# Performance work log

Measured on AMD Instinct MI355X. Metric: run time of the kernel, lower is better.

## Reference

```python
import jax, jax.numpy as jnp
import numpy as np

V, E, H, A, B, S = 32000, 1024, 1024, 1024, 64, 512

def setup_inputs() -> dict:
    key = jax.random.key(0)
    ks = jax.random.split(key, 20)
    sc = lambda d: 1.0 / np.sqrt(d)
    return {
        "x": jax.random.randint(ks[0], (B,), 0, V),
        "encoder_outputs": jax.random.normal(ks[1], (S, B, H), jnp.float32),
        "h0": jax.random.normal(ks[2], (1, B, H), jnp.float32),
        "c0": jax.random.normal(ks[3], (1, B, H), jnp.float32),
        "Wa": jax.random.normal(ks[4], (A, H), jnp.float32) * sc(H),
        "b_wa": jnp.zeros((A,), jnp.float32),
        "Ua": jax.random.normal(ks[5], (A, H), jnp.float32) * sc(H),
        "b_ua": jnp.zeros((A,), jnp.float32),
        "va": jax.random.normal(ks[6], (1, A), jnp.float32) * sc(A),
        "b_va": jnp.zeros((1,), jnp.float32),
        "emb": jax.random.normal(ks[7], (V, E), jnp.float32) * 0.02,
        "W_ih": jax.random.normal(ks[8], (4 * H, E + H), jnp.float32) * sc(E + H),
        "W_hh": jax.random.normal(ks[9], (4 * H, H), jnp.float32) * sc(H),
        "b_ih": jnp.zeros((4 * H,), jnp.float32),
        "b_hh": jnp.zeros((4 * H,), jnp.float32),
        "W_clf": jax.random.normal(ks[10], (V, H), jnp.float32) * sc(H),
        "b_clf": jnp.zeros((V,), jnp.float32),
    }

def reference(x, encoder_outputs, h0, c0, Wa, b_wa, Ua, b_ua, va, b_va, emb,
              W_ih, W_hh, b_ih, b_hh, W_clf, b_clf):
    # Bahdanau additive attention: scores over time (axis 0)
    tmp1 = jnp.einsum('lbh,ah->lba', h0, Wa) + b_wa            # [1,B,A]
    tmp2 = jnp.einsum('sbh,ah->sba', encoder_outputs, Ua) + b_ua  # [S,B,A]
    scores = jnp.einsum('sba,oa->sbo', jnp.tanh(tmp1 + tmp2), va) + b_va  # [S,B,1]
    w = jax.nn.softmax(scores, axis=0)                          # softmax over S
    ctx = jnp.einsum('sb,sbh->bh', w[..., 0], encoder_outputs)  # [B,H]
    # embed token, concat with context
    inp = jnp.concatenate([emb[x], ctx], axis=-1)               # [B,E+H]
    # single LSTM step (PyTorch gate order i,f,g,o)
    gates = inp @ W_ih.T + b_ih + h0[0] @ W_hh.T + b_hh         # [B,4H]
    i, f, g, o = jnp.split(gates, 4, axis=-1)
    c1 = jax.nn.sigmoid(f) * c0[0] + jax.nn.sigmoid(i) * jnp.tanh(g)
    h1 = jax.nn.sigmoid(o) * jnp.tanh(c1)
    logits = h1 @ W_clf.T + b_clf                               # [B,V]
    return jax.nn.log_softmax(logits, axis=-1)[None]            # [1,B,V]
```

## Files before the change

### kernel.cpp

```cpp
#include <hip/hip_runtime.h>
#include <hip/hip_bf16.h>
#include <math.h>

typedef unsigned short u16;
typedef unsigned int u32;
typedef __attribute__((ext_vector_type(4))) float f32x4;
typedef __attribute__((ext_vector_type(8))) short s16x8;
typedef __attribute__((ext_vector_type(8))) unsigned short u16x8;

#define DEV __device__ __forceinline__


DEV u16 f2bf(float f) {
    union { float f; u32 u; } x{f};
    return (u16)((x.u + 0x7FFFu + ((x.u >> 16) & 1u)) >> 16);
}
DEV float bf2f(u16 h) {
    union { u32 u; float f; } x;
    x.u = ((u32)h) << 16;
    return x.f;
}
DEV float sigm(float x) { return 1.0f / (1.0f + __expf(-x)); }
DEV float tanh_f(float x) {
    float c = fminf(fmaxf(x, -9.0f), 9.0f);
    float e = __expf(2.0f * c);
    return (e - 1.0f) / (e + 1.0f);
}

#define GLL16(g, l) __builtin_amdgcn_global_load_lds( \
    (const __attribute__((address_space(1))) u32*)(g), \
    (__attribute__((address_space(3))) u32*)(l), 16, 0, 0)

__global__ __launch_bounds__(256) void kprepcvt(
    const float* __restrict__ enc, const float* __restrict__ Ua,
    const float* __restrict__ h0, u16* __restrict__ encbf,
    u16* __restrict__ Uabf, u16* __restrict__ h0bf, float* __restrict__ scores)
{
    int bid = blockIdx.x, t = threadIdx.x;
    if (bid < 16384) {
        int i = bid * 256 + t;
        float4 f0 = ((const float4*)enc)[i * 2];
        float4 f1 = ((const float4*)enc)[i * 2 + 1];
        u16x8 o = {f2bf(f0.x), f2bf(f0.y), f2bf(f0.z), f2bf(f0.w),
                   f2bf(f1.x), f2bf(f1.y), f2bf(f1.z), f2bf(f1.w)};
        ((u16x8*)encbf)[i] = o;
    } else if (bid < 16400) {
        int i = (bid - 16384) * 2048 + t * 8;
        *(float4*)(scores + i) = (float4){0.f, 0.f, 0.f, 0.f};
        *(float4*)(scores + i + 4) = (float4){0.f, 0.f, 0.f, 0.f};
    } else if (bid < 16912) {
        int i = (bid - 16400) * 256 + t;
        float4 f0 = ((const float4*)Ua)[i * 2];
        float4 f1 = ((const float4*)Ua)[i * 2 + 1];
        u16x8 o = {f2bf(f0.x), f2bf(f0.y), f2bf(f0.z), f2bf(f0.w),
                   f2bf(f1.x), f2bf(f1.y), f2bf(f1.z), f2bf(f1.w)};
        ((u16x8*)Uabf)[i] = o;
    } else {
        int i = (bid - 16912) * 256 + t;
        float4 f0 = ((const float4*)h0)[i * 2];
        float4 f1 = ((const float4*)h0)[i * 2 + 1];
        u16x8 o = {f2bf(f0.x), f2bf(f0.y), f2bf(f0.z), f2bf(f0.w),
                   f2bf(f1.x), f2bf(f1.y), f2bf(f1.z), f2bf(f1.w)};
        ((u16x8*)h0bf)[i] = o;
    }
}


template<int F0>
DEV void mmq(f32x4 (&acc)[8][4], const s16x8 (&af)[2][2], const s16x8 (&bfrag)[4][2]) {
#pragma unroll
    for (int f = 0; f < 2; f++)
#pragma unroll
        for (int j = 0; j < 4; j++) {
            acc[F0 + f][j] = __builtin_amdgcn_mfma_f32_16x16x32_bf16(af[f][0], bfrag[j][0], acc[F0 + f][j], 0, 0, 0);
            acc[F0 + f][j] = __builtin_amdgcn_mfma_f32_16x16x32_bf16(af[f][1], bfrag[j][1], acc[F0 + f][j], 0, 0, 0);
        }
}

__global__ __launch_bounds__(512, 1) void kscores256v2(
    const u16* __restrict__ encbf, const u16* __restrict__ Uabf,
    const float* __restrict__ tmp1c, const float* __restrict__ va,
    float* __restrict__ scores)
{
    __shared__ __align__(16) u16 shm[65536];

    int wg  = blockIdx.x;
    int lin = (wg & 7) * 64 + (wg >> 3);
    int mt  = lin >> 2, nt = lin & 3;

    int t = threadIdx.x;
    int wid = t >> 6, lane = t & 63;
    int wm = wid >> 2, wn = wid & 3;
    int lr = lane & 15, lg = lane >> 4;

    f32x4 acc[8][4];
#pragma unroll
    for (int i = 0; i < 8; i++)
#pragma unroll
        for (int j = 0; j < 4; j++) acc[i][j] = (f32x4){0.f, 0.f, 0.f, 0.f};

    int srow = t >> 3;
    int sq8  = ((t & 7) ^ (srow & 7)) * 8;
    const u16* asrcb = encbf + (size_t)(mt * 256 + srow) * 1024 + sq8;
    const u16* bsrcb = Uabf + (size_t)(nt * 256 + srow) * 1024 + sq8;

#define STG_A(SE, RB, KO) GLL16(asrcb + (size_t)(RB) * 1024 + (KO), shm + (SE) + (RB) * 64 + t * 8)
#define STG_B(SE, RB, KO) GLL16(bsrcb + (size_t)(RB) * 1024 + (KO), shm + (SE) + 16384 + (RB) * 64 + t * 8)

    const u16* Abase = shm + (wm * 128 + lr) * 64;
    const u16* Bbase = shm + 16384 + (wn * 64 + lr) * 64;
    int xor8 = (lr & 7) * 8;
    int o0 = (lg * 8) ^ xor8;
    int o1 = (32 + lg * 8) ^ xor8;

    s16x8 af[2][2], bfrag[4][2];

#define RD_A2(F0, AB) { \
    af[0][0] = *(const s16x8*)((AB) + (F0) * 1024 + o0); \
    af[0][1] = *(const s16x8*)((AB) + (F0) * 1024 + o1); \
    af[1][0] = *(const s16x8*)((AB) + (F0 + 1) * 1024 + o0); \
    af[1][1] = *(const s16x8*)((AB) + (F0 + 1) * 1024 + o1); }

#define MM(F0) \
    __builtin_amdgcn_s_setprio(1); \
    mmq<F0>(acc, af, bfrag); \
    __builtin_amdgcn_s_setprio(0);

#define BAR() \
    __builtin_amdgcn_s_barrier(); \
    __builtin_amdgcn_sched_barrier(0);

    STG_B(0, 0, 0);  STG_B(0, 64, 0);  STG_B(0, 128, 0); STG_B(0, 192, 0);
    STG_A(0, 0, 0);  STG_A(0, 128, 0); STG_A(0, 64, 0);  STG_A(0, 192, 0);
    STG_B(32768, 0, 64);  STG_B(32768, 64, 64);
    STG_B(32768, 128, 64); STG_B(32768, 192, 64);
    STG_A(32768, 0, 64);  STG_A(32768, 128, 64);
    asm volatile("s_waitcnt vmcnt(6)" ::: "memory");
    BAR();

#define TILE_BODY(T, SB, SBX, SAH, STP2, WC) { \
    int kA = (T) * 64 + 128; \
    int kH = (T) * 64 + 64; \
    const u16* Ab = Abase + (SB); \
    const u16* Bb = Bbase + (SB); \
     \
    if (SAH) { STG_A((SBX), 64, kH); STG_A((SBX), 192, kH); } \
    _Pragma("unroll") \
    for (int j = 0; j < 4; j++) { \
        bfrag[j][0] = *(const s16x8*)(Bb + j * 1024 + o0); \
        bfrag[j][1] = *(const s16x8*)(Bb + j * 1024 + o1); \
    } \
    RD_A2(0, Ab); \
    MM(0); \
    BAR();                       \
     \
    if (STP2) { STG_B((SB), 0, kA); STG_B((SB), 64, kA); } \
    RD_A2(2, Ab); \
    MM(2); \
    __builtin_amdgcn_sched_barrier(0); \
     \
    if (STP2) { STG_B((SB), 128, kA); STG_B((SB), 192, kA); } \
    RD_A2(4, Ab); \
    MM(4); \
    BAR();                       \
     \
    if (STP2) { STG_A((SB), 0, kA); STG_A((SB), 128, kA); } \
    RD_A2(6, Ab); \
    if ((WC) == 6) { asm volatile("s_waitcnt vmcnt(6)" ::: "memory"); } \
    else if ((WC) == 0) { asm volatile("s_waitcnt vmcnt(0)" ::: "memory"); } \
    MM(6); \
    BAR();                       \
}

    for (int tt = 0; tt < 7; tt++) {
        int T0 = tt * 2;
        TILE_BODY(T0, 0, 32768, 1, 1, 6);
        TILE_BODY(T0 + 1, 32768, 0, 1, 1, 6);
    }
    TILE_BODY(14, 0, 32768, 1, 0, 0);
    TILE_BODY(15, 32768, 0, 0, 0, -1);

    float* ltmp = (float*)shm;
#pragma unroll
    for (int i = 0; i < 8; i++) {
        int idx = t + i * 512;
        int row = idx >> 6, c4 = idx & 63;
        float4 v = *(const float4*)(tmp1c + row * 1024 + nt * 256 + c4 * 4);
        *(float4*)(ltmp + row * 260 + c4 * 4) = v;
    }
    __syncthreads();

    float vaj[4];
#pragma unroll
    for (int j = 0; j < 4; j++) vaj[j] = va[nt * 256 + wn * 64 + j * 16 + lr];

#pragma unroll
    for (int fi = 0; fi < 8; fi++) {
        float rs[4] = {0.f, 0.f, 0.f, 0.f};
#pragma unroll
        for (int j = 0; j < 4; j++) {
            int ac = wn * 64 + j * 16 + lr;
#pragma unroll
            for (int r = 0; r < 4; r++) {
                int b = (fi * 16 + lg * 4 + r) & 63;
                rs[r] += vaj[j] * tanh_f(acc[fi][j][r] + ltmp[b * 260 + ac]);
            }
        }
#pragma unroll
        for (int m = 1; m < 16; m <<= 1)
#pragma unroll
            for (int r = 0; r < 4; r++) rs[r] += __shfl_xor(rs[r], m, 64);
        if (lr == 0) {
            int mrow = mt * 256 + wm * 128 + fi * 16 + lg * 4;
#pragma unroll
            for (int r = 0; r < 4; r++) atomicAdd(&scores[mrow + r], rs[r]);
        }
    }
#undef STG_A
#undef STG_B
#undef RD_A2
#undef MM
#undef BAR
#undef TILE_BODY
}

__global__ __launch_bounds__(256) void kskinny(
    const u16* __restrict__ Abf, int Ktot,
    const float* __restrict__ B1, int K1,
    const float* __restrict__ B2,
    float* __restrict__ Cout, int N, int klen)
{
    __shared__ u16 As[64 * 40];
    __shared__ u16 Bs[128 * 40];

    int nt = blockIdx.x, p = blockIdx.y;
    int t = threadIdx.x;
    int wid = t >> 6, lane = t & 63;
    int lr = lane & 15, lg = lane >> 4;
    int K2 = Ktot - K1;

    f32x4 acc[4][2];
#pragma unroll
    for (int i = 0; i < 4; i++)
#pragma unroll
        for (int j = 0; j < 2; j++) acc[i][j] = (f32x4){0.f, 0.f, 0.f, 0.f};

    int arow = t >> 2, aq = t & 3;
    const u16* ap = Abf + (size_t)arow * Ktot + aq * 8;
    u16* asw = &As[arow * 40 + aq * 8];

    int brow = t >> 1, bhalf = t & 1;
    int n = nt * 128 + brow;
    u16* bsw = &Bs[brow * 40 + bhalf * 16];

    int kbeg = p * klen, kend = kbeg + klen;
    for (int k0 = kbeg; k0 < kend; k0 += 32) {
        __syncthreads();
        *(uint4*)asw = *(const uint4*)(ap + k0);
        int kk = k0 + bhalf * 16;
        const float* bp = (kk < K1) ? (B1 + (size_t)n * K1 + kk)
                                    : (B2 + (size_t)n * K2 + (kk - K1));
        float4 b0 = ((const float4*)bp)[0];
        float4 b1 = ((const float4*)bp)[1];
        float4 b2 = ((const float4*)bp)[2];
        float4 b3 = ((const float4*)bp)[3];
        u16x8 q0 = {f2bf(b0.x), f2bf(b0.y), f2bf(b0.z), f2bf(b0.w),
                    f2bf(b1.x), f2bf(b1.y), f2bf(b1.z), f2bf(b1.w)};
        u16x8 q1 = {f2bf(b2.x), f2bf(b2.y), f2bf(b2.z), f2bf(b2.w),
                    f2bf(b3.x), f2bf(b3.y), f2bf(b3.z), f2bf(b3.w)};
        *(u16x8*)bsw = q0;
        *(u16x8*)(bsw + 8) = q1;
        __syncthreads();

        const u16* abase = &As[lr * 40 + lg * 8];
        const u16* bbase = &Bs[(wid * 32 + lr) * 40 + lg * 8];
        s16x8 af[4], bfr[2];
#pragma unroll
        for (int i = 0; i < 4; i++) af[i]  = *(const s16x8*)(abase + i * 16 * 40);
#pragma unroll
        for (int j = 0; j < 2; j++) bfr[j] = *(const s16x8*)(bbase + j * 16 * 40);
#pragma unroll
        for (int i = 0; i < 4; i++)
#pragma unroll
            for (int j = 0; j < 2; j++)
                acc[i][j] = __builtin_amdgcn_mfma_f32_16x16x32_bf16(af[i], bfr[j], acc[i][j], 0, 0, 0);
    }

#pragma unroll
    for (int i = 0; i < 4; i++)
#pragma unroll
        for (int j = 0; j < 2; j++) {
            int m = i * 16 + lg * 4;
            int col = nt * 128 + wid * 32 + j * 16 + lr;
#pragma unroll
            for (int r = 0; r < 4; r++)
                Cout[((size_t)(p * 64 + m + r)) * N + col] = acc[i][j][r];
        }
}

__global__ void kredbias(const float* __restrict__ part, const float* __restrict__ bias1,
                         const float* __restrict__ bias2, float* __restrict__ out,
                         int N, int P)
{
    int idx = blockIdx.x * blockDim.x + threadIdx.x;
    if (idx >= 64 * N) return;
    int n = idx % N;
    float v = bias1[n] + bias2[n];
    for (int p = 0; p < P; p++) v += part[(size_t)p * 64 * N + idx];
    out[idx] = v;
}

__global__ __launch_bounds__(128) void kctx(const u16* __restrict__ encbf,
                                            const float* __restrict__ scores,
                                            float* __restrict__ pctx)
{
    int b = blockIdx.x & 63, ch = blockIdx.x >> 6;
    int t = threadIdx.x;
    int lane = t & 63, wv = t >> 6;
    __shared__ float redm[2], reds[2];
    __shared__ float wch[64];

    float v[4];
    float m = -1e30f;
#pragma unroll
    for (int k = 0; k < 4; k++) {
        v[k] = scores[(t + k * 128) * 64 + b];
        m = fmaxf(m, v[k]);
    }
#pragma unroll
    for (int mask = 1; mask < 64; mask <<= 1) m = fmaxf(m, __shfl_xor(m, mask, 64));
    if (lane == 0) redm[wv] = m;
    __syncthreads();
    m = fmaxf(redm[0], redm[1]);
    float e[4], sum = 0.f;
#pragma unroll
    for (int k = 0; k < 4; k++) { e[k] = __expf(v[k] - m); sum += e[k]; }
#pragma unroll
    for (int mask = 1; mask < 64; mask <<= 1) sum += __shfl_xor(sum, mask, 64);
    if (lane == 0) reds[wv] = sum;
    __syncthreads();
    sum = reds[0] + reds[1];
    float inv = 1.0f / sum;
#pragma unroll
    for (int k = 0; k < 4; k++) {
        int s = t + k * 128;
        if ((s >> 6) == ch) wch[s & 63] = e[k] * inv;
    }
    __syncthreads();

    float acc[8] = {0.f, 0.f, 0.f, 0.f, 0.f, 0.f, 0.f, 0.f};
    int s0 = ch * 64;
#pragma unroll 4
    for (int si = 0; si < 64; si++) {
        float wvv = wch[si];
        u16x8 ev = *(const u16x8*)(encbf + ((size_t)((s0 + si) * 64 + b)) * 1024 + t * 8);
#pragma unroll
        for (int k = 0; k < 8; k++) acc[k] += wvv * bf2f(ev[k]);
    }
    float* dst = pctx + ((size_t)(ch * 64 + b)) * 1024 + t * 8;
    *(float4*)dst = (float4){acc[0], acc[1], acc[2], acc[3]};
    *(float4*)(dst + 4) = (float4){acc[4], acc[5], acc[6], acc[7]};
}

__global__ void kbuild(const int* __restrict__ x, const float* __restrict__ emb,
                       const float* __restrict__ pctx, const float* __restrict__ h0,
                       u16* __restrict__ inp2bf)
{
    int idx = blockIdx.x * blockDim.x + threadIdx.x;
    if (idx >= 64 * 3072) return;
    int b = idx / 3072, k = idx % 3072;
    float v;
    if (k < 1024) {
        v = emb[(size_t)x[b] * 1024 + k];
    } else if (k < 2048) {
        int h = k - 1024;
        v = 0.f;
        for (int p = 0; p < 8; p++) v += pctx[(size_t)(p * 64 + b) * 1024 + h];
    } else {
        v = h0[b * 1024 + (k - 2048)];
    }
    inp2bf[idx] = f2bf(v);
}

__global__ void klstm(const float* __restrict__ gp, const float* __restrict__ b_ih,
                      const float* __restrict__ b_hh, const float* __restrict__ c0,
                      u16* __restrict__ h1bf)
{
    int idx = blockIdx.x * blockDim.x + threadIdx.x;
    int b = idx >> 10, j = idx & 1023;
    float ig = b_ih[j] + b_hh[j];
    float fg = b_ih[1024 + j] + b_hh[1024 + j];
    float gg = b_ih[2048 + j] + b_hh[2048 + j];
    float og = b_ih[3072 + j] + b_hh[3072 + j];
    for (int p = 0; p < 8; p++) {
        const float* g = gp + ((size_t)p * 64 + b) * 4096;
        ig += g[j]; fg += g[1024 + j]; gg += g[2048 + j]; og += g[3072 + j];
    }
    float c = sigm(fg) * c0[idx] + sigm(ig) * tanh_f(gg);
    float h = sigm(og) * tanh_f(c);
    h1bf[idx] = f2bf(h);
}

__global__ __launch_bounds__(256) void klsm1(const float* __restrict__ lp,
                                             const float* __restrict__ b_clf,
                                             float* __restrict__ logitsc,
                                             float* __restrict__ mp,
                                             float* __restrict__ sp)
{
    int b = blockIdx.x >> 3, ch = blockIdx.x & 7;
    int t = threadIdx.x;
    int lane = t & 63, wv = t >> 6;
    __shared__ float rm[4], rs[4];
    size_t base = (size_t)b * 32000 + ch * 4000;
    int vbase = ch * 4000;

    float v[16];
    float mx = -1e30f;
#pragma unroll
    for (int i = 0; i < 16; i++) {
        int idx = t + i * 256;
        if (idx < 4000) {
            float s = b_clf[vbase + idx] + lp[base + idx] + lp[2048000 + base + idx];
            v[i] = s;
            mx = fmaxf(mx, s);
        } else v[i] = -1e30f;
    }
#pragma unroll
    for (int mask = 1; mask < 64; mask <<= 1) mx = fmaxf(mx, __shfl_xor(mx, mask, 64));
    if (lane == 0) rm[wv] = mx;
    __syncthreads();
    mx = fmaxf(fmaxf(rm[0], rm[1]), fmaxf(rm[2], rm[3]));
    float s = 0.f;
#pragma unroll
    for (int i = 0; i < 16; i++) {
        int idx = t + i * 256;
        if (idx < 4000) {
            s += __expf(v[i] - mx);
            logitsc[base + idx] = v[i];
        }
    }
#pragma unroll
    for (int mask = 1; mask < 64; mask <<= 1) s += __shfl_xor(s, mask, 64);
    if (lane == 0) rs[wv] = s;
    __syncthreads();
    if (t == 0) {
        mp[blockIdx.x] = mx;
        sp[blockIdx.x] = (rs[0] + rs[1]) + (rs[2] + rs[3]);
    }
}

__global__ __launch_bounds__(256) void klsm2(const float* __restrict__ logitsc,
                                             const float* __restrict__ mp,
                                             const float* __restrict__ sp,
                                             float* __restrict__ out)
{
    int b = blockIdx.x >> 3, ch = blockIdx.x & 7;
    int t = threadIdx.x;
    float m = -1e30f;
#pragma unroll
    for (int k = 0; k < 8; k++) m = fmaxf(m, mp[b * 8 + k]);
    float s = 0.f;
#pragma unroll
    for (int k = 0; k < 8; k++) s += sp[b * 8 + k] * __expf(mp[b * 8 + k] - m);
    float lse = m + logf(s);
    size_t base = (size_t)b * 32000 + ch * 4000;
#pragma unroll
    for (int i = 0; i < 16; i++) {
        int idx = t + i * 256;
        if (idx < 4000) out[base + idx] = logitsc[base + idx] - lse;
    }
}

extern "C" void kernel_launch(void* const* d_in, const int* in_sizes, int n_in,
                              void* d_out, int out_size, void* d_ws, size_t ws_size,
                              hipStream_t stream)
{
    const int*   x     = (const int*)d_in[0];
    const float* enc   = (const float*)d_in[1];
    const float* h0    = (const float*)d_in[2];
    const float* c0    = (const float*)d_in[3];
    const float* Wa    = (const float*)d_in[4];
    const float* b_wa  = (const float*)d_in[5];
    const float* Ua    = (const float*)d_in[6];
    const float* b_ua  = (const float*)d_in[7];
    const float* va    = (const float*)d_in[8];
    const float* emb   = (const float*)d_in[10];
    const float* W_ih  = (const float*)d_in[11];
    const float* W_hh  = (const float*)d_in[12];
    const float* b_ih  = (const float*)d_in[13];
    const float* b_hh  = (const float*)d_in[14];
    const float* W_clf = (const float*)d_in[15];
    const float* b_clf = (const float*)d_in[16];
    float* out = (float*)d_out;

    char* ws = (char*)d_ws;
    u16*   encbf    = (u16*)  (ws + 0);
    float* gparts   = (float*)(ws + 0);
    float* lparts   = (float*)(ws + 8388608);
    float* logitsc  = (float*)(ws + 25165824);
    float* scores   = (float*)(ws + 67108864);
    float* tmp1part = (float*)(ws + 67371008);
    float* tmp1c    = (float*)(ws + 69468160);
    u16*   h0bf     = (u16*)  (ws + 69730304);
    u16*   Uabf     = (u16*)  (ws + 69861376);
    float* pctx     = (float*)(ws + 71958528);
    u16*   inp2bf   = (u16*)  (ws + 74055680);
    u16*   h1bf     = (u16*)  (ws + 74448896);
    float* mp       = (float*)(ws + 74579968);
    float* sp       = (float*)(ws + 74582016);

    kprepcvt<<<16944, 256, 0, stream>>>(enc, Ua, h0, encbf, Uabf, h0bf, scores);

    {
        dim3 g(8, 8);
        kskinny<<<g, 256, 0, stream>>>(h0bf, 1024, Wa, 1024, nullptr, tmp1part, 1024, 128);
    }
    kredbias<<<256, 256, 0, stream>>>(tmp1part, b_wa, b_ua, tmp1c, 1024, 8);

    kscores256v2<<<512, 512, 0, stream>>>(encbf, Uabf, tmp1c, va, scores);
    kctx<<<512, 128, 0, stream>>>(encbf, scores, pctx);
    kbuild<<<768, 256, 0, stream>>>(x, emb, pctx, h0, inp2bf);

    {
        dim3 g(32, 8);
        kskinny<<<g, 256, 0, stream>>>(inp2bf, 3072, W_ih, 2048, W_hh, gparts, 4096, 384);
    }
    klstm<<<256, 256, 0, stream>>>(gparts, b_ih, b_hh, c0, h1bf);

    {
        dim3 g(250, 2);
        kskinny<<<g, 256, 0, stream>>>(h1bf, 1024, W_clf, 1024, nullptr, lparts, 32000, 512);
    }
    klsm1<<<512, 256, 0, stream>>>(lparts, b_clf, logitsc, mp, sp);
    klsm2<<<512, 256, 0, stream>>>(logitsc, mp, sp, out);
}
```

Before: 212.6 us.

## Replace split-K partial buffers with atomic accumulation into bias-initialized outputs

The attention-query and LSTM-gate GEMMs now atomically add their split-K partials into output buffers that the prep kernel pre-fills with the summed biases. This removes the separate reduction kernel and the partial-sum passes in the LSTM kernel. The context kernel likewise atomically accumulates per-chunk contributions into a zeroed sum, so kbuild no longer loops over eight partials. kbuild and klstm are also vectorised, and the cost is atomic contention plus run-to-run non-deterministic summation order.

```diff
diff --git a/kernel.cpp b/kernel.cpp
--- a/kernel.cpp
+++ b/kernel.cpp
@@ -33,8 +33,12 @@
 
 __global__ __launch_bounds__(256) void kprepcvt(
     const float* __restrict__ enc, const float* __restrict__ Ua,
-    const float* __restrict__ h0, u16* __restrict__ encbf,
-    u16* __restrict__ Uabf, u16* __restrict__ h0bf, float* __restrict__ scores)
+    const float* __restrict__ h0, const float* __restrict__ b_wa,
+    const float* __restrict__ b_ua, const float* __restrict__ b_ih,
+    const float* __restrict__ b_hh,
+    u16* __restrict__ encbf, u16* __restrict__ Uabf, u16* __restrict__ h0bf,
+    float* __restrict__ scores, float* __restrict__ tmp1c,
+    float* __restrict__ ctxsum, float* __restrict__ gates)
 {
     int bid = blockIdx.x, t = threadIdx.x;
     if (bid < 16384) {
@@ -55,13 +59,35 @@
         u16x8 o = {f2bf(f0.x), f2bf(f0.y), f2bf(f0.z), f2bf(f0.w),
                    f2bf(f1.x), f2bf(f1.y), f2bf(f1.z), f2bf(f1.w)};
         ((u16x8*)Uabf)[i] = o;
-    } else {
+    } else if (bid < 16944) {
         int i = (bid - 16912) * 256 + t;
         float4 f0 = ((const float4*)h0)[i * 2];
         float4 f1 = ((const float4*)h0)[i * 2 + 1];
         u16x8 o = {f2bf(f0.x), f2bf(f0.y), f2bf(f0.z), f2bf(f0.w),
                    f2bf(f1.x), f2bf(f1.y), f2bf(f1.z), f2bf(f1.w)};
         ((u16x8*)h0bf)[i] = o;
+    } else if (bid < 16976) {
+        int i = (bid - 16944) * 2048 + t * 8;
+        int a = i & 1023;
+        float4 w0 = *(const float4*)(b_wa + a);
+        float4 w1 = *(const float4*)(b_wa + a + 4);
+        float4 u0 = *(const float4*)(b_ua + a);
+        float4 u1 = *(const float4*)(b_ua + a + 4);
+        *(float4*)(tmp1c + i) = (float4){w0.x + u0.x, w0.y + u0.y, w0.z + u0.z, w0.w + u0.w};
+        *(float4*)(tmp1c + i + 4) = (float4){w1.x + u1.x, w1.y + u1.y, w1.z + u1.z, w1.w + u1.w};
+    } else if (bid < 17008) {
+        int i = (bid - 16976) * 2048 + t * 8;
+        *(float4*)(ctxsum + i) = (float4){0.f, 0.f, 0.f, 0.f};
+        *(float4*)(ctxsum + i + 4) = (float4){0.f, 0.f, 0.f, 0.f};
+    } else {
+        int i = (bid - 17008) * 2048 + t * 8;
+        int j = i & 4095;
+        float4 a0 = *(const float4*)(b_ih + j);
+        float4 a1 = *(const float4*)(b_ih + j + 4);
+        float4 c0 = *(const float4*)(b_hh + j);
+        float4 c1 = *(const float4*)(b_hh + j + 4);
+        *(float4*)(gates + i) = (float4){a0.x + c0.x, a0.y + c0.y, a0.z + c0.z, a0.w + c0.w};
+        *(float4*)(gates + i + 4) = (float4){a1.x + c1.x, a1.y + c1.y, a1.z + c1.z, a1.w + c1.w};
     }
 }
 
@@ -228,7 +254,7 @@
     const u16* __restrict__ Abf, int Ktot,
     const float* __restrict__ B1, int K1,
     const float* __restrict__ B2,
-    float* __restrict__ Cout, int N, int klen)
+    float* __restrict__ Cout, int N, int klen, int atomic_mode)
 {
     __shared__ u16 As[64 * 40];
     __shared__ u16 Bs[128 * 40];
@@ -292,27 +318,21 @@
         for (int j = 0; j < 2; j++) {
             int m = i * 16 + lg * 4;
             int col = nt * 128 + wid * 32 + j * 16 + lr;
-#pragma unroll
-            for (int r = 0; r < 4; r++)
-                Cout[((size_t)(p * 64 + m + r)) * N + col] = acc[i][j][r];
+            if (atomic_mode) {
+#pragma unroll
+                for (int r = 0; r < 4; r++)
+                    atomicAdd(&Cout[(size_t)(m + r) * N + col], acc[i][j][r]);
+            } else {
+#pragma unroll
+                for (int r = 0; r < 4; r++)
+                    Cout[((size_t)(p * 64 + m + r)) * N + col] = acc[i][j][r];
+            }
         }
-}
-
-__global__ void kredbias(const float* __restrict__ part, const float* __restrict__ bias1,
-                         const float* __restrict__ bias2, float* __restrict__ out,
-                         int N, int P)
-{
-    int idx = blockIdx.x * blockDim.x + threadIdx.x;
-    if (idx >= 64 * N) return;
-    int n = idx % N;
-    float v = bias1[n] + bias2[n];
-    for (int p = 0; p < P; p++) v += part[(size_t)p * 64 * N + idx];
-    out[idx] = v;
 }
 
 __global__ __launch_bounds__(128) void kctx(const u16* __restrict__ encbf,
                                             const float* __restrict__ scores,
-                                            float* __restrict__ pctx)
+                                            float* __restrict__ ctxsum)
 {
     int b = blockIdx.x & 63, ch = blockIdx.x >> 6;
     int t = threadIdx.x;
@@ -357,48 +377,48 @@
 #pragma unroll
         for (int k = 0; k < 8; k++) acc[k] += wvv * bf2f(ev[k]);
     }
-    float* dst = pctx + ((size_t)(ch * 64 + b)) * 1024 + t * 8;
-    *(float4*)dst = (float4){acc[0], acc[1], acc[2], acc[3]};
-    *(float4*)(dst + 4) = (float4){acc[4], acc[5], acc[6], acc[7]};
-}
-
-__global__ void kbuild(const int* __restrict__ x, const float* __restrict__ emb,
-                       const float* __restrict__ pctx, const float* __restrict__ h0,
-                       u16* __restrict__ inp2bf)
-{
-    int idx = blockIdx.x * blockDim.x + threadIdx.x;
-    if (idx >= 64 * 3072) return;
-    int b = idx / 3072, k = idx % 3072;
-    float v;
-    if (k < 1024) {
-        v = emb[(size_t)x[b] * 1024 + k];
-    } else if (k < 2048) {
-        int h = k - 1024;
-        v = 0.f;
-        for (int p = 0; p < 8; p++) v += pctx[(size_t)(p * 64 + b) * 1024 + h];
-    } else {
-        v = h0[b * 1024 + (k - 2048)];
-    }
-    inp2bf[idx] = f2bf(v);
-}
-
-__global__ void klstm(const float* __restrict__ gp, const float* __restrict__ b_ih,
-                      const float* __restrict__ b_hh, const float* __restrict__ c0,
-                      u16* __restrict__ h1bf)
-{
-    int idx = blockIdx.x * blockDim.x + threadIdx.x;
-    int b = idx >> 10, j = idx & 1023;
-    float ig = b_ih[j] + b_hh[j];
-    float fg = b_ih[1024 + j] + b_hh[1024 + j];
-    float gg = b_ih[2048 + j] + b_hh[2048 + j];
-    float og = b_ih[3072 + j] + b_hh[3072 + j];
-    for (int p = 0; p < 8; p++) {
-        const float* g = gp + ((size_t)p * 64 + b) * 4096;
-        ig += g[j]; fg += g[1024 + j]; gg += g[2048 + j]; og += g[3072 + j];
-    }
-    float c = sigm(fg) * c0[idx] + sigm(ig) * tanh_f(gg);
-    float h = sigm(og) * tanh_f(c);
-    h1bf[idx] = f2bf(h);
+    float* dst = ctxsum + (size_t)b * 1024 + t * 8;
+#pragma unroll
+    for (int k = 0; k < 8; k++) atomicAdd(dst + k, acc[k]);
+}
+
+__global__ __launch_bounds__(256) void kbuild(const int* __restrict__ x,
+                                              const float* __restrict__ emb,
+                                              const float* __restrict__ ctxsum,
+                                              const float* __restrict__ h0,
+                                              u16* __restrict__ inp2bf)
+{
+    int i8 = (blockIdx.x * 256 + threadIdx.x) * 8;
+    int b = i8 / 3072, k = i8 % 3072;
+    const float* src;
+    if (k < 1024)       src = emb + (size_t)x[b] * 1024 + k;
+    else if (k < 2048)  src = ctxsum + (size_t)b * 1024 + (k - 1024);
+    else                src = h0 + (size_t)b * 1024 + (k - 2048);
+    float4 f0 = *(const float4*)src;
+    float4 f1 = *(const float4*)(src + 4);
+    u16x8 o = {f2bf(f0.x), f2bf(f0.y), f2bf(f0.z), f2bf(f0.w),
+               f2bf(f1.x), f2bf(f1.y), f2bf(f1.z), f2bf(f1.w)};
+    *(u16x8*)(inp2bf + i8) = o;
+}
+
+__global__ __launch_bounds__(256) void klstm(const float* __restrict__ g,
+                                             const float* __restrict__ c0,
+                                             u16* __restrict__ h1bf)
+{
+    int i4 = blockIdx.x * 256 + threadIdx.x;
+    int b = i4 >> 8, j4 = (i4 & 255) * 4;
+    const float* gb = g + (size_t)b * 4096;
+    float4 ig = *(const float4*)(gb + j4);
+    float4 fg = *(const float4*)(gb + 1024 + j4);
+    float4 gg = *(const float4*)(gb + 2048 + j4);
+    float4 og = *(const float4*)(gb + 3072 + j4);
+    float4 cv = *(const float4*)(c0 + (size_t)b * 1024 + j4);
+    ushort4 o;
+    o.x = f2bf(sigm(og.x) * tanh_f(sigm(fg.x) * cv.x + sigm(ig.x) * tanh_f(gg.x)));
+    o.y = f2bf(sigm(og.y) * tanh_f(sigm(fg.y) * cv.y + sigm(ig.y) * tanh_f(gg.y)));
+    o.z = f2bf(sigm(og.z) * tanh_f(sigm(fg.z) * cv.z + sigm(ig.z) * tanh_f(gg.z)));
+    o.w = f2bf(sigm(og.w) * tanh_f(sigm(fg.w) * cv.w + sigm(ig.w) * tanh_f(gg.w)));
+    *(ushort4*)(h1bf + (size_t)b * 1024 + j4) = o;
 }
 
 __global__ __launch_bounds__(256) void klsm1(const float* __restrict__ lp,
@@ -495,41 +515,41 @@
 
     char* ws = (char*)d_ws;
     u16*   encbf    = (u16*)  (ws + 0);
-    float* gparts   = (float*)(ws + 0);
     float* lparts   = (float*)(ws + 8388608);
     float* logitsc  = (float*)(ws + 25165824);
     float* scores   = (float*)(ws + 67108864);
-    float* tmp1part = (float*)(ws + 67371008);
-    float* tmp1c    = (float*)(ws + 69468160);
-    u16*   h0bf     = (u16*)  (ws + 69730304);
-    u16*   Uabf     = (u16*)  (ws + 69861376);
-    float* pctx     = (float*)(ws + 71958528);
-    u16*   inp2bf   = (u16*)  (ws + 74055680);
-    u16*   h1bf     = (u16*)  (ws + 74448896);
-    float* mp       = (float*)(ws + 74579968);
-    float* sp       = (float*)(ws + 74582016);
-
-    kprepcvt<<<16944, 256, 0, stream>>>(enc, Ua, h0, encbf, Uabf, h0bf, scores);
+    float* tmp1c    = (float*)(ws + 67239936);
+    u16*   h0bf     = (u16*)  (ws + 67502080);
+    u16*   Uabf     = (u16*)  (ws + 67633152);
+    float* ctxsum   = (float*)(ws + 69730304);
+    u16*   inp2bf   = (u16*)  (ws + 69992448);
+    u16*   h1bf     = (u16*)  (ws + 70385664);
+    float* gates    = (float*)(ws + 70516736);
+    float* mp       = (float*)(ws + 71565312);
+    float* sp       = (float*)(ws + 71567360);
+
+    kprepcvt<<<17136, 256, 0, stream>>>(enc, Ua, h0, b_wa, b_ua, b_ih, b_hh,
+                                        encbf, Uabf, h0bf, scores, tmp1c,
+                                        ctxsum, gates);
 
     {
         dim3 g(8, 8);
-        kskinny<<<g, 256, 0, stream>>>(h0bf, 1024, Wa, 1024, nullptr, tmp1part, 1024, 128);
-    }
-    kredbias<<<256, 256, 0, stream>>>(tmp1part, b_wa, b_ua, tmp1c, 1024, 8);
+        kskinny<<<g, 256, 0, stream>>>(h0bf, 1024, Wa, 1024, nullptr, tmp1c, 1024, 128, 1);
+    }
 
     kscores256v2<<<512, 512, 0, stream>>>(encbf, Uabf, tmp1c, va, scores);
-    kctx<<<512, 128, 0, stream>>>(encbf, scores, pctx);
-    kbuild<<<768, 256, 0, stream>>>(x, emb, pctx, h0, inp2bf);
+    kctx<<<512, 128, 0, stream>>>(encbf, scores, ctxsum);
+    kbuild<<<96, 256, 0, stream>>>(x, emb, ctxsum, h0, inp2bf);
 
     {
         dim3 g(32, 8);
-        kskinny<<<g, 256, 0, stream>>>(inp2bf, 3072, W_ih, 2048, W_hh, gparts, 4096, 384);
-    }
-    klstm<<<256, 256, 0, stream>>>(gparts, b_ih, b_hh, c0, h1bf);
+        kskinny<<<g, 256, 0, stream>>>(inp2bf, 3072, W_ih, 2048, W_hh, gates, 4096, 384, 1);
+    }
+    klstm<<<64, 256, 0, stream>>>(gates, c0, h1bf);
 
     {
         dim3 g(250, 2);
-        kskinny<<<g, 256, 0, stream>>>(h1bf, 1024, W_clf, 1024, nullptr, lparts, 32000, 512);
+        kskinny<<<g, 256, 0, stream>>>(h1bf, 1024, W_clf, 1024, nullptr, lparts, 32000, 512, 0);
     }
     klsm1<<<512, 256, 0, stream>>>(lparts, b_clf, logitsc, mp, sp);
     klsm2<<<512, 256, 0, stream>>>(logitsc, mp, sp, out);
```

After: 228.0 us. 1.07x slower.
